# Kernel tuning notes

Hardware: AMD Instinct MI355X
Metric: run time of the kernel (lower is better)

The kernel has to match this reference:

```python
import jax, jax.numpy as jnp
import numpy as np

N, E, IN_DIM, OUT_DIM = 50000, 800000, 128, 128
NEG_SLOPE = 0.01  # F.leaky_relu default


def gcn_conv(x, W, b, src, dst, n_nodes):
    """PyG GCNConv: symmetric norm with self-loops, linear (no bias) -> aggregate -> +bias.
    Self-loop contribution added analytically (norm = deg_inv_sqrt[i]^2) instead of
    materializing an extended edge list."""
    h = x @ W.T  # [N, out]
    deg = jnp.zeros((n_nodes,), x.dtype).at[dst].add(1.0) + 1.0  # in-degree incl. self-loop
    dis = jax.lax.rsqrt(deg)  # deg^{-1/2}
    norm = dis[src] * dis[dst]  # [E]
    msgs = h[src] * norm[:, None]  # gather + scale, [E, out]
    agg = jax.ops.segment_sum(msgs, dst, num_segments=n_nodes)  # scatter-add
    agg = agg + h * (dis * dis)[:, None]  # self-loop messages
    return agg + b


def setup_inputs() -> dict:
    key = jax.random.key(0)
    ks = jax.random.split(key, 6)
    x = jax.random.normal(ks[0], (N, IN_DIM), jnp.float32)
    edge_index = jax.random.randint(ks[1], (2, E), 0, N, dtype=jnp.int32)
    batch = jnp.zeros((N,), jnp.int32)
    W1 = jax.random.normal(ks[2], (OUT_DIM, IN_DIM), jnp.float32) * (1.0 / np.sqrt(IN_DIM))
    b1 = jnp.zeros((OUT_DIM,), jnp.float32)
    W2 = jax.random.normal(ks[3], (OUT_DIM, OUT_DIM), jnp.float32) * (1.0 / np.sqrt(OUT_DIM))
    b2 = jnp.zeros((OUT_DIM,), jnp.float32)
    return {"x": x, "edge_index": edge_index, "batch": batch,
            "W1": W1, "b1": b1, "W2": W2, "b2": b2}


def reference(x, edge_index, batch, W1, b1, W2, b2):
    src, dst = edge_index[0], edge_index[1]
    n = x.shape[0]
    h = gcn_conv(x, W1, b1, src, dst, n)
    h = jax.nn.leaky_relu(h, NEG_SLOPE)
    # dropout is identity in eval mode (training=False)
    return gcn_conv(h, W2, b2, src, dst, n)
```

## Files before the change

### kernel.cpp

```cpp
#include <hip/hip_runtime.h>
#include <hip/hip_bf16.h>
#include <hip/hip_fp16.h>

#define DIM 128
#define NCHUNK 256
#define XLD 136
#define WLD 136

typedef unsigned short u16;
typedef unsigned int u32;
typedef __attribute__((ext_vector_type(8))) short bf16x8;
typedef __attribute__((ext_vector_type(4))) float f32x4;

__device__ __forceinline__ float bfbits2f(u16 u) {
    return __uint_as_float(((u32)u) << 16);
}
__device__ __forceinline__ u16 f2bf(float f) {
    __hip_bfloat16 b = __float2bfloat16(f);
    return *reinterpret_cast<u16*>(&b);
}
__device__ __forceinline__ u32 pack2bf(float lo, float hi) {
    return (u32)f2bf(lo) | ((u32)f2bf(hi) << 16);
}
__device__ __forceinline__ float h16tof(u16 u) {
    __half hh = *reinterpret_cast<__half*>(&u);
    return __half2float(hh);
}
__device__ __forceinline__ u16 ftoh16(float f) {
    __half hh = __float2half(f);
    return *reinterpret_cast<u16*>(&hh);
}

__global__ __launch_bounds__(256) void k_count(const u16* __restrict__ x,
                                               int* __restrict__ flagp,
                                               const int* __restrict__ dst,
                                               int* __restrict__ counts,
                                               int* __restrict__ rank, int E) {
    if (blockIdx.x == 0 && threadIdx.x == 0) {
        int weird = 0;
        for (int i = 0; i < 256; i += 2) {
            u16 v = x[i];
            int e = (v >> 7) & 0xff;
            if ((v & 0x7fff) != 0 && (e >= 133 || e <= 100)) weird++;
        }
        *flagp = (weird > 16) ? 1 : 0;
    }
    int e = blockIdx.x * blockDim.x + threadIdx.x;
    if (e < E) rank[e] = atomicAdd(&counts[dst[e]], 1);
}

__global__ __launch_bounds__(256) void k_chunksum(const int* __restrict__ counts,
                                                  int* __restrict__ chunksum,
                                                  int N, int chunk) {
    __shared__ int r[256];
    int t = threadIdx.x, b = blockIdx.x;
    int idx = b * chunk + t;
    r[t] = (t < chunk && idx < N) ? counts[idx] : 0;
    __syncthreads();
    for (int off = 128; off > 0; off >>= 1) {
        if (t < off) r[t] += r[t + off];
        __syncthreads();
    }
    if (t == 0) chunksum[b] = r[0];
}

__global__ void k_scanbase(const int* __restrict__ chunksum,
                           int* __restrict__ chunkbase,
                           int* __restrict__ rowptr, int N) {
    if (threadIdx.x == 0 && blockIdx.x == 0) {
        int run = 0;
        for (int i = 0; i < NCHUNK; ++i) { chunkbase[i] = run; run += chunksum[i]; }
        rowptr[N] = run;
    }
}

__global__ __launch_bounds__(256) void k_rowptr(const int* __restrict__ counts,
                                                const int* __restrict__ chunkbase,
                                                int* __restrict__ rowptr,
                                                float* __restrict__ dis,
                                                u32* __restrict__ pay,
                                                int N, int chunk) {
    __shared__ int sc[256];
    int t = threadIdx.x, b = blockIdx.x;
    int idx = b * chunk + t;
    int v = (t < chunk && idx < N) ? counts[idx] : 0;
    sc[t] = v;
    __syncthreads();
    for (int off = 1; off < 256; off <<= 1) {
        int add = (t >= off) ? sc[t - off] : 0;
        __syncthreads();
        sc[t] += add;
        __syncthreads();
    }
    if (t < chunk && idx < N) {
        rowptr[idx] = chunkbase[b] + sc[t] - v;
        float dv = rsqrtf((float)v + 1.0f);
        dis[idx] = dv;
        pay[idx] = ((u32)idx << 16) | (u32)ftoh16(dv);
    }
}

__global__ __launch_bounds__(256) void k_fill(const int* __restrict__ src,
                                              const int* __restrict__ dst,
                                              const int* __restrict__ rowptr,
                                              const int* __restrict__ rank,
                                              const u32* __restrict__ pay,
                                              u32* __restrict__ elist, int E) {
    int e = blockIdx.x * blockDim.x + threadIdx.x;
    if (e < E) {
        int d = dst[e];
        int s = src[e];
        elist[rowptr[d] + rank[e]] = pay[s];
    }
}

__global__ __launch_bounds__(256) void k_gemm(const void* __restrict__ in,
                                              const void* __restrict__ W,
                                              u16* __restrict__ h, int N,
                                              const int* __restrict__ flagp, int in_mode) {
    __shared__ u16 Xs[64 * XLD];
    __shared__ u16 Wsh[128 * WLD];
    const int tid = threadIdx.x;
    const int flag = *flagp;
    const int in_f32 = in_mode ? flag : 0;
    const int n0 = blockIdx.x * 64;

    if (flag) {
        const float* Wf = (const float*)W;
        for (int t = tid; t < 128 * 32; t += 256) {
            int r = t >> 5, c4 = (t & 31) * 4;
            float4 w = *(const float4*)(Wf + r * DIM + c4);
            uint2 pw = make_uint2(pack2bf(w.x, w.y), pack2bf(w.z, w.w));
            *(uint2*)(Wsh + r * WLD + c4) = pw;
        }
    } else {
        const u16* Wu = (const u16*)W;
        for (int t = tid; t < 128 * 16; t += 256) {
            int r = t >> 4, c8 = (t & 15) * 8;
            *(int4*)(Wsh + r * WLD + c8) = *(const int4*)(Wu + r * DIM + c8);
        }
    }
    if (in_f32) {
        const float* xf = (const float*)in;
        for (int t = tid; t < 64 * 32; t += 256) {
            int r = t >> 5, c4 = (t & 31) * 4;
            int n = n0 + r;
            float4 xv = make_float4(0.f, 0.f, 0.f, 0.f);
            if (n < N) xv = *(const float4*)(xf + (size_t)n * DIM + c4);
            uint2 px = make_uint2(pack2bf(xv.x, xv.y), pack2bf(xv.z, xv.w));
            *(uint2*)(Xs + r * XLD + c4) = px;
        }
    } else {
        const u16* xu = (const u16*)in;
        for (int t = tid; t < 64 * 16; t += 256) {
            int r = t >> 4, c8 = (t & 15) * 8;
            int n = n0 + r;
            int4 v = make_int4(0, 0, 0, 0);
            if (n < N) v = *(const int4*)(xu + (size_t)n * DIM + c8);
            *(int4*)(Xs + r * XLD + c8) = v;
        }
    }
    __syncthreads();

    const int wid = tid >> 6;
    const int lane = tid & 63;
    const int m_base = wid * 16;
    const int idx16 = lane & 15;
    const int koff = (lane >> 4) * 8;

    bf16x8 afrag[4];
#pragma unroll
    for (int ks = 0; ks < 4; ++ks)
        afrag[ks] = *(const bf16x8*)(Xs + (m_base + idx16) * XLD + ks * 32 + koff);

    f32x4 acc[8];
#pragma unroll
    for (int ct = 0; ct < 8; ++ct) acc[ct] = (f32x4){0.f, 0.f, 0.f, 0.f};

#pragma unroll
    for (int ct = 0; ct < 8; ++ct) {
#pragma unroll
        for (int ks = 0; ks < 4; ++ks) {
            bf16x8 bfrag = *(const bf16x8*)(Wsh + (ct * 16 + idx16) * WLD + ks * 32 + koff);
            acc[ct] = __builtin_amdgcn_mfma_f32_16x16x32_bf16(afrag[ks], bfrag, acc[ct], 0, 0, 0);
        }
    }

    const int drow = (lane >> 4) * 4;
#pragma unroll
    for (int ct = 0; ct < 8; ++ct) {
#pragma unroll
        for (int r = 0; r < 4; ++r) {
            int row = n0 + m_base + drow + r;
            if (row < N) h[(size_t)row * DIM + ct * 16 + idx16] = f2bf(acc[ct][r]);
        }
    }
}

template <bool RELU, bool OUT_BF16>
__global__ __launch_bounds__(256) void k_agg(const u16* __restrict__ h,
                                             const float* __restrict__ dis,
                                             const int* __restrict__ rowptr,
                                             const u32* __restrict__ elist,
                                             const void* __restrict__ bias,
                                             void* __restrict__ out, int N,
                                             const int* __restrict__ flagp) {
    const int lane = threadIdx.x & 63;
    const int d = blockIdx.x * 4 + (threadIdx.x >> 6);
    if (d >= N) return;
    const int flag = *flagp;
    const int q  = lane >> 4;
    const int cb = (lane & 15) * 8;

    const int start = rowptr[d];
    const int end   = rowptr[d + 1];
    const int last  = end - 1;
    const float dd  = dis[d];

    float acc[8];
#pragma unroll
    for (int k = 0; k < 8; ++k) acc[k] = 0.f;

    for (int j = start; j < end; j += 16) {
        const int i0 = j + q, i1 = i0 + 4, i2 = i0 + 8, i3 = i0 + 12;
        const u32 e0 = elist[i0 <= last ? i0 : last];
        const u32 e1 = elist[i1 <= last ? i1 : last];
        const u32 e2 = elist[i2 <= last ? i2 : last];
        const u32 e3 = elist[i3 <= last ? i3 : last];
        const float w0 = (i0 <= last) ? h16tof((u16)(e0 & 0xffff)) : 0.f;
        const float w1 = (i1 <= last) ? h16tof((u16)(e1 & 0xffff)) : 0.f;
        const float w2 = (i2 <= last) ? h16tof((u16)(e2 & 0xffff)) : 0.f;
        const float w3 = (i3 <= last) ? h16tof((u16)(e3 & 0xffff)) : 0.f;
        const int4 r0 = *(const int4*)(h + ((size_t)(e0 >> 16)) * DIM + cb);
        const int4 r1 = *(const int4*)(h + ((size_t)(e1 >> 16)) * DIM + cb);
        const int4 r2 = *(const int4*)(h + ((size_t)(e2 >> 16)) * DIM + cb);
        const int4 r3 = *(const int4*)(h + ((size_t)(e3 >> 16)) * DIM + cb);
        const u32 v0[4] = {(u32)r0.x, (u32)r0.y, (u32)r0.z, (u32)r0.w};
        const u32 v1[4] = {(u32)r1.x, (u32)r1.y, (u32)r1.z, (u32)r1.w};
        const u32 v2[4] = {(u32)r2.x, (u32)r2.y, (u32)r2.z, (u32)r2.w};
        const u32 v3[4] = {(u32)r3.x, (u32)r3.y, (u32)r3.z, (u32)r3.w};
#pragma unroll
        for (int k = 0; k < 4; ++k) {
            acc[2 * k]     = fmaf(bfbits2f((u16)(v0[k] & 0xffff)), w0, acc[2 * k]);
            acc[2 * k + 1] = fmaf(bfbits2f((u16)(v0[k] >> 16)),    w0, acc[2 * k + 1]);
        }
#pragma unroll
        for (int k = 0; k < 4; ++k) {
            acc[2 * k]     = fmaf(bfbits2f((u16)(v1[k] & 0xffff)), w1, acc[2 * k]);
            acc[2 * k + 1] = fmaf(bfbits2f((u16)(v1[k] >> 16)),    w1, acc[2 * k + 1]);
        }
#pragma unroll
        for (int k = 0; k < 4; ++k) {
            acc[2 * k]     = fmaf(bfbits2f((u16)(v2[k] & 0xffff)), w2, acc[2 * k]);
            acc[2 * k + 1] = fmaf(bfbits2f((u16)(v2[k] >> 16)),    w2, acc[2 * k + 1]);
        }
#pragma unroll
        for (int k = 0; k < 4; ++k) {
            acc[2 * k]     = fmaf(bfbits2f((u16)(v3[k] & 0xffff)), w3, acc[2 * k]);
            acc[2 * k + 1] = fmaf(bfbits2f((u16)(v3[k] >> 16)),    w3, acc[2 * k + 1]);
        }
    }

#pragma unroll
    for (int k = 0; k < 8; ++k) {
        acc[k] += __shfl_xor(acc[k], 16, 64);
        acc[k] += __shfl_xor(acc[k], 32, 64);
    }

    if (q != 0) return;

    const float d2 = dd * dd;
    int4 rs = *(const int4*)(h + (size_t)d * DIM + cb);
    u32 vs[4] = {(u32)rs.x, (u32)rs.y, (u32)rs.z, (u32)rs.w};
    float res[8];
#pragma unroll
    for (int k = 0; k < 4; ++k) {
        res[2 * k]     = fmaf(bfbits2f((u16)(vs[k] & 0xffff)), d2, acc[2 * k] * dd);
        res[2 * k + 1] = fmaf(bfbits2f((u16)(vs[k] >> 16)),    d2, acc[2 * k + 1] * dd);
    }
    if (flag) {
        const float* bf = (const float*)bias;
#pragma unroll
        for (int k = 0; k < 8; ++k) res[k] += bf[cb + k];
    } else {
        const u16* bu = (const u16*)bias;
#pragma unroll
        for (int k = 0; k < 8; ++k) res[k] += bfbits2f(bu[cb + k]);
    }
    if (RELU) {
#pragma unroll
        for (int k = 0; k < 8; ++k) res[k] = res[k] > 0.f ? res[k] : 0.01f * res[k];
    }
    if (OUT_BF16) {
        u32 pk[4];
#pragma unroll
        for (int k = 0; k < 4; ++k) pk[k] = pack2bf(res[2 * k], res[2 * k + 1]);
        *(int4*)((u16*)out + (size_t)d * DIM + cb) = make_int4(pk[0], pk[1], pk[2], pk[3]);
    } else {
        float* op = (float*)out + (size_t)d * DIM + cb;
        *(float4*)op       = make_float4(res[0], res[1], res[2], res[3]);
        *(float4*)(op + 4) = make_float4(res[4], res[5], res[6], res[7]);
    }
}

extern "C" void kernel_launch(void* const* d_in, const int* in_sizes, int n_in,
                              void* d_out, int out_size, void* d_ws, size_t ws_size,
                              hipStream_t stream) {
    const void* x  = d_in[0];
    const int*  ei = (const int*)d_in[1];
    const void* W1 = d_in[3];
    const void* b1 = d_in[4];
    const void* W2 = d_in[5];
    const void* b2 = d_in[6];

    const int N = in_sizes[0] / DIM;
    const int E = in_sizes[1] / 2;
    const int* src = ei;
    const int* dst = ei + E;
    const int chunk = (N + NCHUNK - 1) / NCHUNK;

    char* ws = (char*)d_ws;
    size_t o = 0;
    int*   flagp    = (int*)(ws + o);   o += 256;
    float* dis      = (float*)(ws + o); o += (((size_t)N * 4 + 255) & ~(size_t)255);
    int*   counts   = (int*)(ws + o);   o += (((size_t)N * 4 + 255) & ~(size_t)255);
    int*   rowptr   = (int*)(ws + o);   o += (((size_t)(N + 1) * 4 + 255) & ~(size_t)255);
    u32*   pay      = (u32*)(ws + o);   o += (((size_t)N * 4 + 255) & ~(size_t)255);
    int*   chunksum = (int*)(ws + o);   o += 1024;
    int*   chunkbase= (int*)(ws + o);   o += 1024;
    int*   rank     = (int*)(ws + o);   o += (((size_t)E * 4 + 255) & ~(size_t)255);
    u32*   elist    = (u32*)(ws + o);   o += (((size_t)E * 4 + 255) & ~(size_t)255);
    u16*   h        = (u16*)(ws + o);

    const int eblk = (E + 255) / 256;
    const int gblk = (N + 63) / 64;
    const int ablk = (N + 3) / 4;

    hipMemsetAsync(counts, 0, (size_t)N * 4, stream);
    k_count<<<eblk, 256, 0, stream>>>((const u16*)x, flagp, dst, counts, rank, E);
    k_chunksum<<<NCHUNK, 256, 0, stream>>>(counts, chunksum, N, chunk);
    k_scanbase<<<1, 64, 0, stream>>>(chunksum, chunkbase, rowptr, N);
    k_rowptr<<<NCHUNK, 256, 0, stream>>>(counts, chunkbase, rowptr, dis, pay, N, chunk);
    k_fill<<<eblk, 256, 0, stream>>>(src, dst, rowptr, rank, pay, elist, E);

    u16* act = (u16*)d_out;

    k_gemm<<<gblk, 256, 0, stream>>>(x, W1, h, N, flagp, 1);
    k_agg<true, true><<<ablk, 256, 0, stream>>>(h, dis, rowptr, elist, b1, act, N, flagp);

    k_gemm<<<gblk, 256, 0, stream>>>(act, W2, h, N, flagp, 0);
    k_agg<false, false><<<ablk, 256, 0, stream>>>(h, dis, rowptr, elist, b2, d_out, N, flagp);
}
```

Baseline: 246.3 us.

## Fold self-loops into CSR, drop rank array, load GEMM A-fragments directly

Result: slower. 251.6 us (+2.2%).

```diff
diff --git a/kernel.cpp b/kernel.cpp
--- a/kernel.cpp
+++ b/kernel.cpp
@@ -4,7 +4,6 @@
 
 #define DIM 128
 #define NCHUNK 256
-#define XLD 136
 #define WLD 136
 
 typedef unsigned short u16;
@@ -34,8 +33,7 @@
 __global__ __launch_bounds__(256) void k_count(const u16* __restrict__ x,
                                                int* __restrict__ flagp,
                                                const int* __restrict__ dst,
-                                               int* __restrict__ counts,
-                                               int* __restrict__ rank, int E) {
+                                               int* __restrict__ counts, int E) {
     if (blockIdx.x == 0 && threadIdx.x == 0) {
         int weird = 0;
         for (int i = 0; i < 256; i += 2) {
@@ -46,7 +44,7 @@
         *flagp = (weird > 16) ? 1 : 0;
     }
     int e = blockIdx.x * blockDim.x + threadIdx.x;
-    if (e < E) rank[e] = atomicAdd(&counts[dst[e]], 1);
+    if (e < E) atomicAdd(&counts[dst[e]], 1);
 }
 
 __global__ __launch_bounds__(256) void k_chunksum(const int* __restrict__ counts,
@@ -55,7 +53,7 @@
     __shared__ int r[256];
     int t = threadIdx.x, b = blockIdx.x;
     int idx = b * chunk + t;
-    r[t] = (t < chunk && idx < N) ? counts[idx] : 0;
+    r[t] = (t < chunk && idx < N) ? counts[idx] + 1 : 0;
     __syncthreads();
     for (int off = 128; off > 0; off >>= 1) {
         if (t < off) r[t] += r[t + off];
@@ -64,17 +62,25 @@
     if (t == 0) chunksum[b] = r[0];
 }
 
-__global__ void k_scanbase(const int* __restrict__ chunksum,
-                           int* __restrict__ chunkbase,
-                           int* __restrict__ rowptr, int N) {
-    if (threadIdx.x == 0 && blockIdx.x == 0) {
-        int run = 0;
-        for (int i = 0; i < NCHUNK; ++i) { chunkbase[i] = run; run += chunksum[i]; }
-        rowptr[N] = run;
-    }
-}
-
-__global__ __launch_bounds__(256) void k_rowptr(const int* __restrict__ counts,
+__global__ __launch_bounds__(256) void k_scanbase(const int* __restrict__ chunksum,
+                                                  int* __restrict__ chunkbase,
+                                                  int* __restrict__ rowptr, int N) {
+    __shared__ int sc[256];
+    int t = threadIdx.x;
+    int v = chunksum[t];
+    sc[t] = v;
+    __syncthreads();
+    for (int off = 1; off < 256; off <<= 1) {
+        int add = (t >= off) ? sc[t - off] : 0;
+        __syncthreads();
+        sc[t] += add;
+        __syncthreads();
+    }
+    chunkbase[t] = sc[t] - v;
+    if (t == 255) rowptr[N] = sc[255];
+}
+
+__global__ __launch_bounds__(256) void k_rowptr(int* __restrict__ counts,
                                                 const int* __restrict__ chunkbase,
                                                 int* __restrict__ rowptr,
                                                 float* __restrict__ dis,
@@ -83,7 +89,7 @@
     __shared__ int sc[256];
     int t = threadIdx.x, b = blockIdx.x;
     int idx = b * chunk + t;
-    int v = (t < chunk && idx < N) ? counts[idx] : 0;
+    int v = (t < chunk && idx < N) ? counts[idx] + 1 : 0;
     sc[t] = v;
     __syncthreads();
     for (int off = 1; off < 256; off <<= 1) {
@@ -94,23 +100,28 @@
     }
     if (t < chunk && idx < N) {
         rowptr[idx] = chunkbase[b] + sc[t] - v;
-        float dv = rsqrtf((float)v + 1.0f);
+        float dv = rsqrtf((float)v);
         dis[idx] = dv;
         pay[idx] = ((u32)idx << 16) | (u32)ftoh16(dv);
+        counts[idx] = 0;
     }
 }
 
 __global__ __launch_bounds__(256) void k_fill(const int* __restrict__ src,
                                               const int* __restrict__ dst,
                                               const int* __restrict__ rowptr,
-                                              const int* __restrict__ rank,
+                                              int* __restrict__ cursor,
                                               const u32* __restrict__ pay,
-                                              u32* __restrict__ elist, int E) {
+                                              u32* __restrict__ elist, int E, int N) {
     int e = blockIdx.x * blockDim.x + threadIdx.x;
     if (e < E) {
         int d = dst[e];
-        int s = src[e];
-        elist[rowptr[d] + rank[e]] = pay[s];
+        int r = atomicAdd(&cursor[d], 1);
+        elist[rowptr[d] + r] = pay[src[e]];
+    } else if (e < E + N) {
+        int d = e - E;
+        int r = atomicAdd(&cursor[d], 1);
+        elist[rowptr[d] + r] = pay[d];
     }
 }
 
@@ -118,7 +129,6 @@
                                               const void* __restrict__ W,
                                               u16* __restrict__ h, int N,
                                               const int* __restrict__ flagp, int in_mode) {
-    __shared__ u16 Xs[64 * XLD];
     __shared__ u16 Wsh[128 * WLD];
     const int tid = threadIdx.x;
     const int flag = *flagp;
@@ -140,38 +150,42 @@
             *(int4*)(Wsh + r * WLD + c8) = *(const int4*)(Wu + r * DIM + c8);
         }
     }
-    if (in_f32) {
-        const float* xf = (const float*)in;
-        for (int t = tid; t < 64 * 32; t += 256) {
-            int r = t >> 5, c4 = (t & 31) * 4;
-            int n = n0 + r;
-            float4 xv = make_float4(0.f, 0.f, 0.f, 0.f);
-            if (n < N) xv = *(const float4*)(xf + (size_t)n * DIM + c4);
-            uint2 px = make_uint2(pack2bf(xv.x, xv.y), pack2bf(xv.z, xv.w));
-            *(uint2*)(Xs + r * XLD + c4) = px;
-        }
-    } else {
-        const u16* xu = (const u16*)in;
-        for (int t = tid; t < 64 * 16; t += 256) {
-            int r = t >> 4, c8 = (t & 15) * 8;
-            int n = n0 + r;
-            int4 v = make_int4(0, 0, 0, 0);
-            if (n < N) v = *(const int4*)(xu + (size_t)n * DIM + c8);
-            *(int4*)(Xs + r * XLD + c8) = v;
-        }
-    }
-    __syncthreads();
 
     const int wid = tid >> 6;
     const int lane = tid & 63;
     const int m_base = wid * 16;
     const int idx16 = lane & 15;
     const int koff = (lane >> 4) * 8;
+    const int n = n0 + m_base + idx16;
 
     bf16x8 afrag[4];
-#pragma unroll
-    for (int ks = 0; ks < 4; ++ks)
-        afrag[ks] = *(const bf16x8*)(Xs + (m_base + idx16) * XLD + ks * 32 + koff);
+    if (in_f32) {
+        const float* xf = (const float*)in;
+#pragma unroll
+        for (int ks = 0; ks < 4; ++ks) {
+            if (n < N) {
+                const float* p = xf + (size_t)n * DIM + ks * 32 + koff;
+                float4 a = *(const float4*)p;
+                float4 b = *(const float4*)(p + 4);
+                union { bf16x8 v8; u32 w[4]; } cv;
+                cv.w[0] = pack2bf(a.x, a.y);
+                cv.w[1] = pack2bf(a.z, a.w);
+                cv.w[2] = pack2bf(b.x, b.y);
+                cv.w[3] = pack2bf(b.z, b.w);
+                afrag[ks] = cv.v8;
+            } else {
+                afrag[ks] = (bf16x8)0;
+            }
+        }
+    } else {
+        const u16* xu = (const u16*)in;
+#pragma unroll
+        for (int ks = 0; ks < 4; ++ks) {
+            afrag[ks] = (n < N) ? *(const bf16x8*)(xu + (size_t)n * DIM + ks * 32 + koff)
+                                : (bf16x8)0;
+        }
+    }
+    __syncthreads();
 
     f32x4 acc[8];
 #pragma unroll
@@ -269,15 +283,9 @@
 
     if (q != 0) return;
 
-    const float d2 = dd * dd;
-    int4 rs = *(const int4*)(h + (size_t)d * DIM + cb);
-    u32 vs[4] = {(u32)rs.x, (u32)rs.y, (u32)rs.z, (u32)rs.w};
     float res[8];
 #pragma unroll
-    for (int k = 0; k < 4; ++k) {
-        res[2 * k]     = fmaf(bfbits2f((u16)(vs[k] & 0xffff)), d2, acc[2 * k] * dd);
-        res[2 * k + 1] = fmaf(bfbits2f((u16)(vs[k] >> 16)),    d2, acc[2 * k + 1] * dd);
-    }
+    for (int k = 0; k < 8; ++k) res[k] = acc[k] * dd;
     if (flag) {
         const float* bf = (const float*)bias;
 #pragma unroll
@@ -328,20 +336,20 @@
     u32*   pay      = (u32*)(ws + o);   o += (((size_t)N * 4 + 255) & ~(size_t)255);
     int*   chunksum = (int*)(ws + o);   o += 1024;
     int*   chunkbase= (int*)(ws + o);   o += 1024;
-    int*   rank     = (int*)(ws + o);   o += (((size_t)E * 4 + 255) & ~(size_t)255);
-    u32*   elist    = (u32*)(ws + o);   o += (((size_t)E * 4 + 255) & ~(size_t)255);
+    u32*   elist    = (u32*)(ws + o);   o += (((size_t)(E + N) * 4 + 255) & ~(size_t)255);
     u16*   h        = (u16*)(ws + o);
 
     const int eblk = (E + 255) / 256;
+    const int fblk = (E + N + 255) / 256;
     const int gblk = (N + 63) / 64;
     const int ablk = (N + 3) / 4;
 
     hipMemsetAsync(counts, 0, (size_t)N * 4, stream);
-    k_count<<<eblk, 256, 0, stream>>>((const u16*)x, flagp, dst, counts, rank, E);
+    k_count<<<eblk, 256, 0, stream>>>((const u16*)x, flagp, dst, counts, E);
     k_chunksum<<<NCHUNK, 256, 0, stream>>>(counts, chunksum, N, chunk);
-    k_scanbase<<<1, 64, 0, stream>>>(chunksum, chunkbase, rowptr, N);
+    k_scanbase<<<1, 256, 0, stream>>>(chunksum, chunkbase, rowptr, N);
     k_rowptr<<<NCHUNK, 256, 0, stream>>>(counts, chunkbase, rowptr, dis, pay, N, chunk);
-    k_fill<<<eblk, 256, 0, stream>>>(src, dst, rowptr, rank, pay, elist, E);
+    k_fill<<<fblk, 256, 0, stream>>>(src, dst, rowptr, counts, pay, elist, E, N);
 
     u16* act = (u16*)d_out;
 
```
